# Kernel optimization log

Measured on AMD Instinct MI355X. Metric: run time of the kernel, lower is better.

Reference implementation:

```python
import jax, jax.numpy as jnp
import numpy as np

NV = 40962      # vertices at mesh level 6 (10*4^6 + 2)
NV_PREV = 10242 # vertices at mesh level 5
GROUPS = 32
EPS = 1e-5


def setup_inputs() -> dict:
    key = jax.random.key(0)
    ks = jax.random.split(key, 8)
    B, Cin, Cout, K = 8, 64, 64, 7
    x = jax.random.normal(ks[0], (B, Cin, NV_PREV), dtype=jnp.float32)
    L_val = jax.random.normal(ks[1], (NV, K), dtype=jnp.float32)
    EW_val = jax.random.normal(ks[2], (NV, K), dtype=jnp.float32)
    NS_val = jax.random.normal(ks[3], (NV, K), dtype=jnp.float32)
    coeffs = jax.random.normal(ks[4], (Cout, Cin, 4), dtype=jnp.float32) * 0.05
    bias = jax.random.normal(ks[5], (Cout,), dtype=jnp.float32) * 0.05
    gamma = jnp.ones((Cout,), dtype=jnp.float32)
    beta = jnp.zeros((Cout,), dtype=jnp.float32)
    nbr_idx = jax.random.randint(ks[6], (NV, K), 0, NV, dtype=jnp.int32)
    return {"x": x, "L_val": L_val, "EW_val": EW_val, "NS_val": NS_val,
            "coeffs": coeffs, "bias": bias, "gamma": gamma, "beta": beta,
            "nbr_idx": nbr_idx}


def reference(x, L_val, EW_val, NS_val, coeffs, bias, gamma, beta, nbr_idx):
    B, Cin, nvp = x.shape
    nv = nbr_idx.shape[0]
    # --- MeshConvTranspose: zero-pad upsample (old vertices are a prefix) ---
    up = jnp.zeros((B, Cin, nv), x.dtype).at[:, :, :nvp].set(x)
    # --- irregular neighbor gather: [B, Cin, nv, 7] ---
    g = up[:, :, nbr_idx]
    # sparse operator applications (shared gather, three weighted sums)
    lap = jnp.einsum('bcvk,vk->bcv', g, L_val)
    ew = jnp.einsum('bcvk,vk->bcv', g, EW_val)
    ns = jnp.einsum('bcvk,vk->bcv', g, NS_val)
    feat = jnp.stack([up, lap, ew, ns], axis=2)  # [B, Cin, 4, nv]
    # learned linear combination over (in_channels, 4 operators)
    out = jnp.einsum('oik,bikv->bov', coeffs, feat) + bias[None, :, None]
    # --- GroupNorm(32, Cout) ---
    Cout = out.shape[1]
    og = out.reshape(B, GROUPS, (Cout // GROUPS) * nv)
    mean = og.mean(axis=-1, keepdims=True)
    var = og.var(axis=-1, keepdims=True)
    og = (og - mean) * jax.lax.rsqrt(var + EPS)
    out = og.reshape(B, Cout, nv) * gamma[None, :, None] + beta[None, :, None]
    # --- ReLU ---
    return jax.nn.relu(out)
```

## Files before the change

### kernel.cpp

```cpp
#include <hip/hip_runtime.h>
#include <hip/hip_bf16.h>

#define NVV    40962
#define NVP    10242
#define BB     8
#define CIN    64
#define COUT   64
#define KK     7
#define EPSV   1e-5f

#define VT      64
#define NTILE   641
#define KDIM    256
#define PSTRIDE 41024

#define CW_OFF  2048
#define XT_OFF  36864
#define PRE_OFF 10524672

typedef __attribute__((ext_vector_type(8))) short short8;
typedef __attribute__((ext_vector_type(4))) float floatx4;

__device__ __forceinline__ unsigned f2bf(float f) {
    unsigned u = __builtin_bit_cast(unsigned, f);
    return (u + 0x7FFFu + ((u >> 16) & 1u)) >> 16;
}
__device__ __forceinline__ unsigned pk2(float a, float b) {
    __hip_bfloat162 h = __float22bfloat162_rn(make_float2(a, b));
    unsigned r;
    __builtin_memcpy(&r, &h, 4);
    return r;
}
__device__ __forceinline__ float bflo(unsigned u) { return __builtin_bit_cast(float, u << 16); }
__device__ __forceinline__ float bfhi(unsigned u) { return __builtin_bit_cast(float, u & 0xffff0000u); }

__global__ __launch_bounds__(256) void k_tr(const float* __restrict__ x,
                                            unsigned short* __restrict__ xT,
                                            const float* __restrict__ coeffs,
                                            unsigned short* __restrict__ cW,
                                            float* __restrict__ stats) {
    __shared__ float tile[64][65];
    const int b    = blockIdx.y;
    const int v0   = blockIdx.x * 64;
    const int lane = threadIdx.x & 63;
    const int wave = threadIdx.x >> 6;
    const int v    = v0 + lane;
    #pragma unroll
    for (int r = 0; r < 16; ++r) {
        int i = wave * 16 + r;
        tile[i][lane] = (v < NVP) ? x[((size_t)b * CIN + i) * NVP + v] : 0.f;
    }
    if (blockIdx.x == 0 && b == 0) {
        for (int t = threadIdx.x; t < 512; t += 256) stats[t] = 0.f;
        for (int t = threadIdx.x; t < COUT * KDIM; t += 256)
            cW[t] = (unsigned short)f2bf(coeffs[t]);
    }
    __syncthreads();
    const int i2 = lane & 31;
    #pragma unroll
    for (int r = 0; r < 8; ++r) {
        int vv = wave * 16 + 2 * r + (lane >> 5);
        if (v0 + vv < NVP) {
            unsigned w = pk2(tile[2 * i2][vv], tile[2 * i2 + 1][vv]);
            ((unsigned*)(xT + ((size_t)b * NVP + v0 + vv) * 64))[i2] = w;
        }
    }
}

__global__ __launch_bounds__(256, 4) void k_conv(
    const unsigned short* __restrict__ xT,
    const float* __restrict__ Lw,
    const float* __restrict__ Ew,
    const float* __restrict__ Nw,
    const unsigned short* __restrict__ cW,
    const float* __restrict__ bias,
    const int*   __restrict__ nbr,
    unsigned short* __restrict__ pre,
    float* __restrict__ stats)
{
    __shared__ unsigned short Fbuf[VT * 256];
    __shared__ float sred[4][4][4];

    const int bid   = blockIdx.x;
    const int b     = bid & 7;
    const int tile  = bid >> 3;
    const int vbase = tile * VT;
    const int tid   = threadIdx.x;
    const int wave  = tid >> 6;
    const int lane  = tid & 63;
    const int q     = lane >> 4;
    const int l15   = lane & 15;

    {
        const int v  = lane;
        const int ic = wave;
        const int vg = vbase + v;
        const bool va = (vg < NVV);
        int jj[KK]; float wl[KK], we[KK], wn[KK];
        #pragma unroll
        for (int k = 0; k < KK; ++k) { jj[k] = NVP; wl[k] = we[k] = wn[k] = 0.f; }
        if (va) {
            #pragma unroll
            for (int k = 0; k < KK; ++k) {
                jj[k] = nbr[vg * KK + k];
                wl[k] = Lw[vg * KK + k];
                we[k] = Ew[vg * KK + k];
                wn[k] = Nw[vg * KK + k];
            }
        }
        const unsigned short* xTb = xT + (size_t)b * NVP * 64 + ic * 16;

        uint4 ga[KK], gb[KK], gu0, gu1;
        gu0 = gu1 = make_uint4(0, 0, 0, 0);
        #pragma unroll
        for (int k = 0; k < KK; ++k) { ga[k] = make_uint4(0,0,0,0); gb[k] = make_uint4(0,0,0,0); }
        if (vg < NVP) {
            const uint4* p = (const uint4*)(xTb + (size_t)vg * 64);
            gu0 = p[0]; gu1 = p[1];
        }
        #pragma unroll
        for (int k = 0; k < KK; ++k) {
            if (jj[k] < NVP) {
                const uint4* p = (const uint4*)(xTb + (size_t)jj[k] * 64);
                ga[k] = p[0]; gb[k] = p[1];
            }
        }

        float l[16], e[16], n[16];
        #pragma unroll
        for (int t = 0; t < 16; ++t) { l[t] = e[t] = n[t] = 0.f; }
        #pragma unroll
        for (int k = 0; k < KK; ++k) {
            const float a = wl[k], bb2 = we[k], c2 = wn[k];
            const unsigned uu[8] = { ga[k].x, ga[k].y, ga[k].z, ga[k].w,
                                     gb[k].x, gb[k].y, gb[k].z, gb[k].w };
            #pragma unroll
            for (int j2 = 0; j2 < 8; ++j2) {
                float f0 = bflo(uu[j2]), f1 = bfhi(uu[j2]);
                l[2*j2]   = fmaf(f0, a,  l[2*j2]);   e[2*j2]   = fmaf(f0, bb2, e[2*j2]);   n[2*j2]   = fmaf(f0, c2, n[2*j2]);
                l[2*j2+1] = fmaf(f1, a,  l[2*j2+1]); e[2*j2+1] = fmaf(f1, bb2, e[2*j2+1]); n[2*j2+1] = fmaf(f1, c2, n[2*j2+1]);
            }
        }
        const unsigned uup[8] = { gu0.x, gu0.y, gu0.z, gu0.w, gu1.x, gu1.y, gu1.z, gu1.w };
        #pragma unroll
        for (int jg = 0; jg < 8; ++jg) {
            const int i0 = 2 * jg;
            uint4 w;
            w.x = pk2(bflo(uup[jg]), l[i0]);
            w.y = pk2(e[i0],   n[i0]);
            w.z = pk2(bfhi(uup[jg]) , l[i0+1]);
            w.w = pk2(e[i0+1], n[i0+1]);
            const int g    = ic * 8 + jg;
            const int phys = g ^ (v & 31);
            *(uint4*)(Fbuf + v * 256 + phys * 8) = w;
        }
    }
    __syncthreads();

    short8 afrag[8];
    {
        const unsigned short* wrow = cW + (16 * wave + l15) * KDIM + q * 8;
        #pragma unroll
        for (int k0 = 0; k0 < 8; ++k0)
            afrag[k0] = *(const short8*)(wrow + k0 * 32);
    }

    floatx4 acc[4] = {{0,0,0,0},{0,0,0,0},{0,0,0,0},{0,0,0,0}};
    #pragma unroll
    for (int k0 = 0; k0 < 8; ++k0) {
        #pragma unroll
        for (int nt = 0; nt < 4; ++nt) {
            const int row  = nt * 16 + l15;
            const int phys = (k0 * 4 + q) ^ (row & 31);
            const short8 bfrag = *(const short8*)(Fbuf + row * 256 + phys * 8);
            acc[nt] = __builtin_amdgcn_mfma_f32_16x16x32_bf16(afrag[k0], bfrag, acc[nt], 0, 0, 0);
        }
    }

    float bs[4];
    #pragma unroll
    for (int r = 0; r < 4; ++r) bs[r] = bias[16 * wave + q * 4 + r];

    float cv[4][4];
    float sA = 0.f, s2A = 0.f, sB = 0.f, s2B = 0.f;
    #pragma unroll
    for (int nt = 0; nt < 4; ++nt) {
        const bool ok = (vbase + nt * 16 + l15 < NVV);
        #pragma unroll
        for (int r = 0; r < 4; ++r) {
            float c = acc[nt][r] + bs[r];
            cv[nt][r] = c;
            if (ok) {
                if (r < 2) { sA += c; s2A = fmaf(c, c, s2A); }
                else       { sB += c; s2B = fmaf(c, c, s2B); }
            }
        }
    }
    #pragma unroll
    for (int m = 1; m < 16; m <<= 1) {
        sA  += __shfl_xor(sA,  m);
        s2A += __shfl_xor(s2A, m);
        sB  += __shfl_xor(sB,  m);
        s2B += __shfl_xor(s2B, m);
    }
    if (l15 == 0) {
        sred[wave][q][0] = sA; sred[wave][q][1] = s2A;
        sred[wave][q][2] = sB; sred[wave][q][3] = s2B;
    }
    __syncthreads();

    float* outT = (float*)Fbuf;
    #pragma unroll
    for (int nt = 0; nt < 4; ++nt)
        #pragma unroll
        for (int r = 0; r < 4; ++r)
            outT[(16 * wave + 4 * q + r) * 68 + nt * 16 + l15] = cv[nt][r];
    __syncthreads();

    {
        const int oo2  = lane >> 5;
        const int vloc = 2 * (lane & 31);
        if (vbase + vloc < NVV) {
            unsigned short* prow = pre + (size_t)(b * COUT + 16 * wave) * PSTRIDE + vbase;
            #pragma unroll
            for (int ot = 0; ot < 8; ++ot) {
                const int oo = 2 * ot + oo2;
                float2 t = *(const float2*)(outT + (16 * wave + oo) * 68 + vloc);
                *(unsigned*)(prow + (size_t)oo * PSTRIDE + vloc) = pk2(t.x, t.y);
            }
        }
    }

    if (tid < 64) {
        const int w = tid >> 4, qq = (tid >> 2) & 3, e = tid & 3;
        const int g = 8 * w + 2 * qq + (e >> 1);
        atomicAdd(&stats[b * 64 + 2 * g + (e & 1)], sred[w][qq][e]);
    }
}

__global__ __launch_bounds__(256) void k_norm(
    const unsigned short* __restrict__ pre,
    float* __restrict__ out,
    const float* __restrict__ stats,
    const float* __restrict__ gamma,
    const float* __restrict__ beta)
{
    const int blk     = blockIdx.x;
    const int b       = blk & 7;
    const int rest    = blk >> 3;
    const int o       = rest & 63;
    const int quarter = rest >> 6;
    const int row     = b * 64 + o;
    const int g = o >> 1;
    const float inv_cnt = 1.f / (float)(2 * NVV);
    const float mean = stats[b * 64 + 2 * g] * inv_cnt;
    const float var  = fmaf(stats[b * 64 + 2 * g + 1], inv_cnt, -mean * mean);
    const float rs   = rsqrtf(var + EPSV);
    const float sc   = gamma[o] * rs;
    const float sh   = fmaf(-mean, sc, beta[o]);

    const uint4* src = (const uint4*)(pre + (size_t)row * PSTRIDE);
    float* orow = out + (size_t)row * NVV;
    #pragma unroll
    for (int it = 0; it < 5; ++it) {
        const int c = quarter * 1280 + it * 256 + (int)threadIdx.x;
        uint4 u = src[c];
        float f[8] = { bflo(u.x), bfhi(u.x), bflo(u.y), bfhi(u.y),
                       bflo(u.z), bfhi(u.z), bflo(u.w), bfhi(u.w) };
        float* p = orow + 8 * c;
        #pragma unroll
        for (int t = 0; t < 4; ++t) {
            float y0 = fmaf(f[2*t],   sc, sh);
            float y1 = fmaf(f[2*t+1], sc, sh);
            float2 v2 = make_float2(y0 > 0.f ? y0 : 0.f, y1 > 0.f ? y1 : 0.f);
            *(float2*)(p + 2 * t) = v2;
        }
    }
    if (quarter == 3 && threadIdx.x == 0) {
        unsigned u = *(const unsigned*)(pre + (size_t)row * PSTRIDE + 40960);
        float y0 = fmaf(bflo(u), sc, sh);
        float y1 = fmaf(bfhi(u), sc, sh);
        *(float2*)(orow + 40960) = make_float2(y0 > 0.f ? y0 : 0.f, y1 > 0.f ? y1 : 0.f);
    }
}

extern "C" void kernel_launch(void* const* d_in, const int* in_sizes, int n_in,
                              void* d_out, int out_size, void* d_ws, size_t ws_size,
                              hipStream_t stream) {
    const float* x      = (const float*)d_in[0];
    const float* Lw     = (const float*)d_in[1];
    const float* Ew     = (const float*)d_in[2];
    const float* Nw     = (const float*)d_in[3];
    const float* coeffs = (const float*)d_in[4];
    const float* bias   = (const float*)d_in[5];
    const float* gamma  = (const float*)d_in[6];
    const float* beta   = (const float*)d_in[7];
    const int*   nbr    = (const int*)d_in[8];
    float* out = (float*)d_out;
    float*          stats = (float*)d_ws;
    unsigned short* cW    = (unsigned short*)((char*)d_ws + CW_OFF);
    unsigned short* xT    = (unsigned short*)((char*)d_ws + XT_OFF);
    unsigned short* pre   = (unsigned short*)((char*)d_ws + PRE_OFF);

    k_tr<<<dim3(161, BB), dim3(256), 0, stream>>>(x, xT, coeffs, cW, stats);

    k_conv<<<dim3(BB * NTILE), dim3(256), 0, stream>>>(xT, Lw, Ew, Nw, cW, bias, nbr, pre, stats);

    k_norm<<<dim3(4 * BB * COUT), dim3(256), 0, stream>>>(pre, out, stats, gamma, beta);
}
```

Baseline: 210.2 us.

## Pack neighbor indices and weights into uint4 and remap gather lanes

The transpose kernel now interleaves each neighbor index with its three operator weights into a single 16-byte record, so the conv kernel fetches per-vertex metadata with vector loads instead of four separate scalar streams. The gather phase is also remapped: each lane now owns 8 channels of one vertex, so 8 adjacent lanes read one full 128-byte xT row per neighbor instead of each lane issuing two 16-byte loads per neighbor. This is meant to improve coalescing of the irregular gathers and cut metadata load instructions. The cost is an extra workspace buffer, a write of about 4.6 MB per call, and each lane now handles two vertices.

```diff
diff --git a/kernel.cpp b/kernel.cpp
--- a/kernel.cpp
+++ b/kernel.cpp
@@ -17,6 +17,7 @@
 #define CW_OFF  2048
 #define XT_OFF  36864
 #define PRE_OFF 10524672
+#define W4_OFF  52533248
 
 typedef __attribute__((ext_vector_type(8))) short short8;
 typedef __attribute__((ext_vector_type(4))) float floatx4;
@@ -38,13 +39,31 @@
                                             unsigned short* __restrict__ xT,
                                             const float* __restrict__ coeffs,
                                             unsigned short* __restrict__ cW,
-                                            float* __restrict__ stats) {
+                                            float* __restrict__ stats,
+                                            const float* __restrict__ Lw,
+                                            const float* __restrict__ Ew,
+                                            const float* __restrict__ Nw,
+                                            const int*   __restrict__ nbr,
+                                            uint4* __restrict__ W4) {
     __shared__ float tile[64][65];
     const int b    = blockIdx.y;
     const int v0   = blockIdx.x * 64;
     const int lane = threadIdx.x & 63;
     const int wave = threadIdx.x >> 6;
     const int v    = v0 + lane;
+
+    {
+        const int gid = (blockIdx.y * 161 + blockIdx.x) * 256 + (int)threadIdx.x;
+        if (gid < NVV * KK) {
+            uint4 qd;
+            qd.x = (unsigned)nbr[gid];
+            qd.y = __builtin_bit_cast(unsigned, Lw[gid]);
+            qd.z = __builtin_bit_cast(unsigned, Ew[gid]);
+            qd.w = __builtin_bit_cast(unsigned, Nw[gid]);
+            W4[gid] = qd;
+        }
+    }
+
     #pragma unroll
     for (int r = 0; r < 16; ++r) {
         int i = wave * 16 + r;
@@ -69,12 +88,9 @@
 
 __global__ __launch_bounds__(256, 4) void k_conv(
     const unsigned short* __restrict__ xT,
-    const float* __restrict__ Lw,
-    const float* __restrict__ Ew,
-    const float* __restrict__ Nw,
+    const uint4* __restrict__ W4,
     const unsigned short* __restrict__ cW,
     const float* __restrict__ bias,
-    const int*   __restrict__ nbr,
     unsigned short* __restrict__ pre,
     float* __restrict__ stats)
 {
@@ -92,67 +108,70 @@
     const int l15   = lane & 15;
 
     {
-        const int v  = lane;
-        const int ic = wave;
-        const int vg = vbase + v;
-        const bool va = (vg < NVV);
-        int jj[KK]; float wl[KK], we[KK], wn[KK];
-        #pragma unroll
-        for (int k = 0; k < KK; ++k) { jj[k] = NVP; wl[k] = we[k] = wn[k] = 0.f; }
-        if (va) {
+        const int c  = lane >> 3;
+        const int vs = lane & 7;
+        const unsigned short* xTb = xT + (size_t)b * NVP * 64;
+
+        uint4 wq[2][7];
+        #pragma unroll
+        for (int r = 0; r < 2; ++r) {
+            const int vg = vbase + r * 32 + wave * 8 + vs;
+            if (vg < NVV) {
+                const uint4* wp = W4 + (size_t)vg * KK;
+                #pragma unroll
+                for (int k = 0; k < KK; ++k) wq[r][k] = wp[k];
+            } else {
+                #pragma unroll
+                for (int k = 0; k < KK; ++k) wq[r][k] = make_uint4(NVP, 0u, 0u, 0u);
+            }
+        }
+
+        #pragma unroll
+        for (int r = 0; r < 2; ++r) {
+            const int vloc = r * 32 + wave * 8 + vs;
+            const int vg   = vbase + vloc;
+
+            uint4 gu = make_uint4(0, 0, 0, 0);
+            if (vg < NVP)
+                gu = *(const uint4*)(xTb + (size_t)vg * 64 + c * 8);
+
+            uint4 gk[KK];
             #pragma unroll
             for (int k = 0; k < KK; ++k) {
-                jj[k] = nbr[vg * KK + k];
-                wl[k] = Lw[vg * KK + k];
-                we[k] = Ew[vg * KK + k];
-                wn[k] = Nw[vg * KK + k];
-            }
-        }
-        const unsigned short* xTb = xT + (size_t)b * NVP * 64 + ic * 16;
-
-        uint4 ga[KK], gb[KK], gu0, gu1;
-        gu0 = gu1 = make_uint4(0, 0, 0, 0);
-        #pragma unroll
-        for (int k = 0; k < KK; ++k) { ga[k] = make_uint4(0,0,0,0); gb[k] = make_uint4(0,0,0,0); }
-        if (vg < NVP) {
-            const uint4* p = (const uint4*)(xTb + (size_t)vg * 64);
-            gu0 = p[0]; gu1 = p[1];
-        }
-        #pragma unroll
-        for (int k = 0; k < KK; ++k) {
-            if (jj[k] < NVP) {
-                const uint4* p = (const uint4*)(xTb + (size_t)jj[k] * 64);
-                ga[k] = p[0]; gb[k] = p[1];
-            }
-        }
-
-        float l[16], e[16], n[16];
-        #pragma unroll
-        for (int t = 0; t < 16; ++t) { l[t] = e[t] = n[t] = 0.f; }
-        #pragma unroll
-        for (int k = 0; k < KK; ++k) {
-            const float a = wl[k], bb2 = we[k], c2 = wn[k];
-            const unsigned uu[8] = { ga[k].x, ga[k].y, ga[k].z, ga[k].w,
-                                     gb[k].x, gb[k].y, gb[k].z, gb[k].w };
-            #pragma unroll
-            for (int j2 = 0; j2 < 8; ++j2) {
-                float f0 = bflo(uu[j2]), f1 = bfhi(uu[j2]);
-                l[2*j2]   = fmaf(f0, a,  l[2*j2]);   e[2*j2]   = fmaf(f0, bb2, e[2*j2]);   n[2*j2]   = fmaf(f0, c2, n[2*j2]);
-                l[2*j2+1] = fmaf(f1, a,  l[2*j2+1]); e[2*j2+1] = fmaf(f1, bb2, e[2*j2+1]); n[2*j2+1] = fmaf(f1, c2, n[2*j2+1]);
-            }
-        }
-        const unsigned uup[8] = { gu0.x, gu0.y, gu0.z, gu0.w, gu1.x, gu1.y, gu1.z, gu1.w };
-        #pragma unroll
-        for (int jg = 0; jg < 8; ++jg) {
-            const int i0 = 2 * jg;
-            uint4 w;
-            w.x = pk2(bflo(uup[jg]), l[i0]);
-            w.y = pk2(e[i0],   n[i0]);
-            w.z = pk2(bfhi(uup[jg]) , l[i0+1]);
-            w.w = pk2(e[i0+1], n[i0+1]);
-            const int g    = ic * 8 + jg;
-            const int phys = g ^ (v & 31);
-            *(uint4*)(Fbuf + v * 256 + phys * 8) = w;
+                const int j = (int)wq[r][k].x;
+                gk[k] = (j < NVP) ? *(const uint4*)(xTb + (size_t)j * 64 + c * 8)
+                                  : make_uint4(0, 0, 0, 0);
+            }
+
+            float l[8], e[8], n[8];
+            #pragma unroll
+            for (int t = 0; t < 8; ++t) { l[t] = e[t] = n[t] = 0.f; }
+            #pragma unroll
+            for (int k = 0; k < KK; ++k) {
+                const float a   = __builtin_bit_cast(float, wq[r][k].y);
+                const float bb2 = __builtin_bit_cast(float, wq[r][k].z);
+                const float c2  = __builtin_bit_cast(float, wq[r][k].w);
+                const unsigned uu[4] = { gk[k].x, gk[k].y, gk[k].z, gk[k].w };
+                #pragma unroll
+                for (int j2 = 0; j2 < 4; ++j2) {
+                    float f0 = bflo(uu[j2]), f1 = bfhi(uu[j2]);
+                    l[2*j2]   = fmaf(f0, a,  l[2*j2]);   e[2*j2]   = fmaf(f0, bb2, e[2*j2]);   n[2*j2]   = fmaf(f0, c2, n[2*j2]);
+                    l[2*j2+1] = fmaf(f1, a,  l[2*j2+1]); e[2*j2+1] = fmaf(f1, bb2, e[2*j2+1]); n[2*j2+1] = fmaf(f1, c2, n[2*j2+1]);
+                }
+            }
+
+            const unsigned uup[4] = { gu.x, gu.y, gu.z, gu.w };
+            #pragma unroll
+            for (int j = 0; j < 4; ++j) {
+                uint4 w;
+                w.x = pk2(bflo(uup[j]), l[2*j]);
+                w.y = pk2(e[2*j],   n[2*j]);
+                w.z = pk2(bfhi(uup[j]), l[2*j+1]);
+                w.w = pk2(e[2*j+1], n[2*j+1]);
+                const int g    = c * 4 + j;
+                const int phys = g ^ (vloc & 31);
+                *(uint4*)(Fbuf + vloc * 256 + phys * 8) = w;
+            }
         }
     }
     __syncthreads();
@@ -188,11 +207,11 @@
         const bool ok = (vbase + nt * 16 + l15 < NVV);
         #pragma unroll
         for (int r = 0; r < 4; ++r) {
-            float c = acc[nt][r] + bs[r];
-            cv[nt][r] = c;
+            float cc = acc[nt][r] + bs[r];
+            cv[nt][r] = cc;
             if (ok) {
-                if (r < 2) { sA += c; s2A = fmaf(c, c, s2A); }
-                else       { sB += c; s2B = fmaf(c, c, s2B); }
+                if (r < 2) { sA += cc; s2A = fmaf(cc, cc, s2A); }
+                else       { sB += cc; s2B = fmaf(cc, cc, s2B); }
             }
         }
     }
@@ -301,10 +320,11 @@
     unsigned short* cW    = (unsigned short*)((char*)d_ws + CW_OFF);
     unsigned short* xT    = (unsigned short*)((char*)d_ws + XT_OFF);
     unsigned short* pre   = (unsigned short*)((char*)d_ws + PRE_OFF);
-
-    k_tr<<<dim3(161, BB), dim3(256), 0, stream>>>(x, xT, coeffs, cW, stats);
-
-    k_conv<<<dim3(BB * NTILE), dim3(256), 0, stream>>>(xT, Lw, Ew, Nw, cW, bias, nbr, pre, stats);
+    uint4*          W4    = (uint4*)((char*)d_ws + W4_OFF);
+
+    k_tr<<<dim3(161, BB), dim3(256), 0, stream>>>(x, xT, coeffs, cW, stats, Lw, Ew, Nw, nbr, W4);
+
+    k_conv<<<dim3(BB * NTILE), dim3(256), 0, stream>>>(xT, W4, cW, bias, pre, stats);
 
     k_norm<<<dim3(4 * BB * COUT), dim3(256), 0, stream>>>(pre, out, stats, gamma, beta);
 }
```

New measurement: 327.7 us. 1.56x slower.
